# Performance work log

Measured on AMD Instinct MI355X. Metric: run time of the kernel, lower is better.

Reference implementation:

```python
import jax, jax.numpy as jnp
import numpy as np

N_HEADS = 16
HEAD_DIM = 64
N_EMBD = 1024
B, S = 2, 2048


def setup_inputs() -> dict:
    key = jax.random.key(0)
    k1, k2, k3 = jax.random.split(key, 3)
    x = jax.random.normal(k1, (B, S, N_EMBD), dtype=jnp.float32)
    W_attn = jax.random.normal(k2, (N_EMBD, 3 * N_EMBD), dtype=jnp.float32) * 0.02
    b_attn = jnp.zeros((3 * N_EMBD,), dtype=jnp.float32)
    W_proj = jax.random.normal(k3, (N_EMBD, N_EMBD), dtype=jnp.float32) * 0.02
    b_proj = jnp.zeros((N_EMBD,), dtype=jnp.float32)
    return {"x": x, "W_attn": W_attn, "b_attn": b_attn, "W_proj": W_proj, "b_proj": b_proj}


def reference(x, W_attn, b_attn, W_proj, b_proj):
    b, s, _ = x.shape
    qkv = x @ W_attn + b_attn  # (b, s, 3*n_embd)
    q, k, v = jnp.split(qkv, 3, axis=-1)
    # (b, s, n_embd) -> (b, h, s, d)
    def heads(t):
        return t.reshape(b, s, N_HEADS, HEAD_DIM).transpose(0, 2, 1, 3)
    q, k, v = heads(q), heads(k), heads(v)
    scale = 1.0 / jnp.sqrt(jnp.float32(HEAD_DIM))
    scores = jnp.einsum("bhqd,bhkd->bhqk", q, k) * scale
    causal = jnp.triu(jnp.full((s, s), -jnp.inf, dtype=scores.dtype), k=1)
    scores = scores + causal[None, None, :, :]
    attn = jax.nn.softmax(scores, axis=-1)
    out = jnp.einsum("bhqk,bhkd->bhqd", attn, v)  # (b, h, s, d)
    out = out.transpose(0, 2, 1, 3).reshape(b, s, N_EMBD)
    return out @ W_proj + b_proj
```

## Files before the change

### kernel.cpp

```cpp
#include <hip/hip_runtime.h>
#include <hip/hip_bf16.h>
#include <stdint.h>
#include <stddef.h>

typedef __bf16 bf16_t;
typedef __attribute__((ext_vector_type(8))) __bf16 bf16x8;
typedef __attribute__((ext_vector_type(4))) __bf16 bf16x4;
typedef __attribute__((ext_vector_type(4))) float f32x4;

#define MFMA_BF16(a, b, c) __builtin_amdgcn_mfma_f32_16x16x32_bf16((a), (b), (c), 0, 0, 0)

__global__ __launch_bounds__(256) void prep(const void* __restrict__ x,
                                            const void* __restrict__ Wa,
                                            const void* __restrict__ Wp,
                                            bf16_t* __restrict__ xb,
                                            bf16_t* __restrict__ Wat,
                                            bf16_t* __restrict__ Wpt,
                                            int* __restrict__ flag) {
  __shared__ int dcnt;
  __shared__ bf16_t tile[32][33];

  const int tid = threadIdx.x;
  if (tid == 0) dcnt = 0;
  __syncthreads();
  {
    const unsigned short* p = (const unsigned short*)x + tid * 16;
    int local = 0;
#pragma unroll
    for (int i = 0; i < 16; ++i) {
      const int e = (p[i] >> 7) & 0xFF;
      if (e >= 0x8D) local++;
    }
    if (local) atomicAdd(&dcnt, local);
  }
  __syncthreads();
  const int isF32 = (dcnt > 4) ? 1 : 0;

  const int b = blockIdx.x;
  if (b == 0 && tid == 0) *flag = isF32;

  if (b < 2048) {
    if (!isF32) return;
    const size_t i = ((size_t)b * 256 + tid) * 8;
    const float4 a0 = *(const float4*)((const float*)x + i);
    const float4 a1 = *(const float4*)((const float*)x + i + 4);
    bf16x8 r;
    r[0] = (__bf16)a0.x; r[1] = (__bf16)a0.y; r[2] = (__bf16)a0.z; r[3] = (__bf16)a0.w;
    r[4] = (__bf16)a1.x; r[5] = (__bf16)a1.y; r[6] = (__bf16)a1.z; r[7] = (__bf16)a1.w;
    *(bf16x8*)(xb + i) = r;
    return;
  }

  const void* in;
  bf16_t* out;
  int R, C, bx, by;
  if (b < 5120) {
    const int idx = b - 2048;
    in = Wa; out = Wat; R = 1024; C = 3072;
    bx = idx % 96; by = idx / 96;
  } else {
    const int idx = b - 5120;
    in = Wp; out = Wpt; R = 1024; C = 1024;
    bx = idx & 31; by = idx >> 5;
  }
  const int tx = tid & 31, ty = tid >> 5;
  const int r0 = by * 32, c0 = bx * 32;
#pragma unroll
  for (int i = 0; i < 4; ++i) {
    const size_t idx2 = (size_t)(r0 + ty + i * 8) * C + (c0 + tx);
    tile[ty + i * 8][tx] = isF32 ? (bf16_t)((const float*)in)[idx2]
                                 : ((const bf16_t*)in)[idx2];
  }
  __syncthreads();
#pragma unroll
  for (int i = 0; i < 4; ++i)
    out[(size_t)(c0 + ty + i * 8) * R + (r0 + tx)] = tile[tx][ty + i * 8];
}

#define GP 72
template <int MODE>
__global__ __launch_bounds__(256) void gemm_bt(const void* A0,
                        const bf16_t* __restrict__ xb,
                        const bf16_t* __restrict__ Bt,
                        const void* __restrict__ bias,
                        void* C,
                        bf16_t* __restrict__ Qs,
                        bf16_t* __restrict__ Kb,
                        bf16_t* __restrict__ dout_bf,
                        int M, int N, int K,
                        const int* __restrict__ flagp) {
  const int isF32 = *flagp;
  const bf16_t* A = (MODE == 1 && isF32) ? xb : (const bf16_t*)A0;
  bf16_t* Vt = dout_bf + (isF32 ? (size_t)4194304 : 0);

  __shared__ __align__(16) unsigned char pool[128 * GP * 2 * 2];
  bf16_t* As = (bf16_t*)pool;
  bf16_t* Bs = (bf16_t*)pool + 128 * GP;

  const int tid = threadIdx.x;
  const int w = tid >> 6, lane = tid & 63;
  const int quad = lane >> 4, l16 = lane & 15;
  const int wm = w >> 1, wn = w & 1;
  const int m0 = blockIdx.y * 128, n0 = blockIdx.x * 128;

  auto loadA = [&](int k0, int it) -> bf16x8 {
    const int g = it * 256 + tid;
    const int row = g >> 3, col = (g & 7) * 8;
    const int m = m0 + row;
    if (MODE == 2) {
      const size_t aoff =
          ((size_t)((m >> 11) * 16 + (k0 >> 6)) * 2048 + (m & 2047)) * 64 + col;
      return *(const bf16x8*)(A + aoff);
    }
    return *(const bf16x8*)(A + (size_t)m * K + (k0 + col));
  };
  auto loadB = [&](int k0, int it) -> bf16x8 {
    const int g = it * 256 + tid;
    const int row = g >> 3, col = (g & 7) * 8;
    return *(const bf16x8*)(Bt + (size_t)(n0 + row) * K + (k0 + col));
  };

  f32x4 acc[4][4];
#pragma unroll
  for (int i = 0; i < 4; ++i)
#pragma unroll
    for (int j = 0; j < 4; ++j) acc[i][j] = f32x4{0.f, 0.f, 0.f, 0.f};

  bf16x8 va[4], vb[4];
#pragma unroll
  for (int it = 0; it < 4; ++it) { va[it] = loadA(0, it); vb[it] = loadB(0, it); }

  for (int k0 = 0; k0 < K; k0 += 64) {
    __syncthreads();
#pragma unroll
    for (int it = 0; it < 4; ++it) {
      const int g = it * 256 + tid;
      const int row = g >> 3, col = (g & 7) * 8;
      *(bf16x8*)&As[row * GP + col] = va[it];
      *(bf16x8*)&Bs[row * GP + col] = vb[it];
    }
    __syncthreads();

    if (k0 + 64 < K) {
#pragma unroll
      for (int it = 0; it < 4; ++it) { va[it] = loadA(k0 + 64, it); vb[it] = loadB(k0 + 64, it); }
    }

#pragma unroll
    for (int kc = 0; kc < 2; ++kc) {
      bf16x8 af[4], bfr[4];
#pragma unroll
      for (int i = 0; i < 4; ++i)
        af[i] = *(const bf16x8*)&As[(wm * 64 + i * 16 + l16) * GP + kc * 32 + quad * 8];
#pragma unroll
      for (int j = 0; j < 4; ++j)
        bfr[j] = *(const bf16x8*)&Bs[(wn * 64 + j * 16 + l16) * GP + kc * 32 + quad * 8];
#pragma unroll
      for (int i = 0; i < 4; ++i)
#pragma unroll
        for (int j = 0; j < 4; ++j) acc[i][j] = MFMA_BF16(af[i], bfr[j], acc[i][j]);
    }
  }

  if (MODE == 1 && n0 >= 2048) {
    bf16_t* tp = (bf16_t*)pool;
    __syncthreads();
#pragma unroll
    for (int j = 0; j < 4; ++j) {
      const int n_l = wn * 64 + j * 16 + l16;
      const int n = n0 + n_l;
      const float bj = isF32 ? ((const float*)bias)[n] : (float)((const bf16_t*)bias)[n];
#pragma unroll
      for (int i = 0; i < 4; ++i) {
#pragma unroll
        for (int r = 0; r < 4; ++r) {
          const int m_l = wm * 64 + i * 16 + quad * 4 + r;
          tp[n_l * 136 + m_l] = (bf16_t)(acc[i][j][r] + bj);
        }
      }
    }
    __syncthreads();
    const int b = m0 >> 11, s0 = m0 & 2047;
#pragma unroll
    for (int seg = 0; seg < 8; ++seg) {
      const int idx = seg * 256 + tid;
      const int n_l = idx >> 4, ms = (idx & 15) * 8;
      const bf16x8 v8 = *(const bf16x8*)&tp[n_l * 136 + ms];
      const int e = (n0 + n_l) & 1023, h = e >> 6, d = e & 63;
      *(bf16x8*)(Vt + ((size_t)(b * 16 + h) * 64 + d) * 2048 + s0 + ms) = v8;
    }
    return;
  }

  if (MODE == 1) {
    bf16_t* tp = (bf16_t*)pool;
    __syncthreads();
    const bool isQ = (n0 < 1024);
    const float sc = isQ ? 0.18033688011f : 1.0f;
#pragma unroll
    for (int j = 0; j < 4; ++j) {
      const int n_l = wn * 64 + j * 16 + l16;
      const int n = n0 + n_l;
      const float bj = isF32 ? ((const float*)bias)[n] : (float)((const bf16_t*)bias)[n];
#pragma unroll
      for (int i = 0; i < 4; ++i) {
#pragma unroll
        for (int r = 0; r < 4; ++r) {
          const int m_l = wm * 64 + i * 16 + quad * 4 + r;
          tp[m_l * 136 + n_l] = (bf16_t)((acc[i][j][r] + bj) * sc);
        }
      }
    }
    __syncthreads();
    bf16_t* dst = isQ ? Qs : Kb;
#pragma unroll
    for (int seg = 0; seg < 8; ++seg) {
      const int idx = seg * 256 + tid;
      const int m_l = idx >> 4, ns = (idx & 15) * 8;
      const bf16x8 v8 = *(const bf16x8*)&tp[m_l * 136 + ns];
      const int m = m0 + m_l;
      const int e = (n0 + ns) & 1023, h = e >> 6, d = e & 63;
      const int bb = m >> 11, s = m & 2047;
      *(bf16x8*)(dst + (((size_t)(bb * 16 + h) * 2048 + s) * 64 + d)) = v8;
    }
    return;
  }

#pragma unroll
  for (int j = 0; j < 4; ++j) {
    const int n = n0 + wn * 64 + j * 16 + l16;
    const float bj = isF32 ? ((const float*)bias)[n] : (float)((const bf16_t*)bias)[n];
#pragma unroll
    for (int i = 0; i < 4; ++i) {
      const int mbase = m0 + wm * 64 + i * 16 + quad * 4;
#pragma unroll
      for (int r = 0; r < 4; ++r) {
        const int m = mbase + r;
        const float v = acc[i][j][r] + bj;
        if (isF32) ((float*)C)[(size_t)m * N + n] = v;
        else       ((bf16_t*)C)[(size_t)m * N + n] = (bf16_t)v;
      }
    }
  }
}

#define AP 72
#define PSP 72
__global__ __launch_bounds__(256, 5) void attn_kernel(bf16_t* QO,
                                                      const bf16_t* __restrict__ Kb,
                                                      const bf16_t* __restrict__ dout_bf,
                                                      const int* __restrict__ flagp) {
  const int isF32 = *flagp;
  const bf16_t* Vt = dout_bf + (isF32 ? (size_t)4194304 : 0);

  __shared__ __align__(16) bf16_t Ks[64 * AP];
  __shared__ __align__(16) bf16_t Vs[64 * AP];
  __shared__ __align__(16) bf16_t Ps[4][16 * PSP];

  const int bid = blockIdx.x;
  const int g = bid >> 5, bh = bid & 31;
  const int qt = (g < 16) ? (31 - g) : (g - 16);

  const int tid = threadIdx.x, w = tid >> 6, lane = tid & 63;
  const int quad = lane >> 4, l16 = lane & 15;

  bf16_t* Q = QO + (size_t)bh * 2048 * 64;
  const bf16_t* K = Kb + (size_t)bh * 2048 * 64;
  const bf16_t* V = Vt + (size_t)bh * 64 * 2048;

  const int qrow = qt * 64 + w * 16;
  const int nkt = qt + 1;

  bf16x8 qf[2];
#pragma unroll
  for (int kk = 0; kk < 2; ++kk)
    qf[kk] = *(const bf16x8*)(Q + (size_t)(qrow + l16) * 64 + kk * 32 + quad * 8);

  f32x4 oacc[4];
  float lsum = 0.f;
#pragma unroll
  for (int jd = 0; jd < 4; ++jd) oacc[jd] = f32x4{0.f, 0.f, 0.f, 0.f};

  const int srow8 = lane >> 3;
  const int scol8 = (lane & 7) * 8;

  auto loadK = [&](int kt, int it) -> bf16x8 {
    const int row = (w + it * 4) * 8 + srow8;
    return *(const bf16x8*)(K + (size_t)(kt * 64 + row) * 64 + scol8);
  };
  auto loadV = [&](int kt, int it) -> bf16x8 {
    const int row = (w + it * 4) * 8 + srow8;
    return *(const bf16x8*)(V + (size_t)row * 2048 + kt * 64 + scol8);
  };

  bf16x8 kv[2], vv[2];
#pragma unroll
  for (int it = 0; it < 2; ++it) { kv[it] = loadK(0, it); vv[it] = loadV(0, it); }

  for (int kt = 0; kt < nkt; ++kt) {
    __syncthreads();
#pragma unroll
    for (int it = 0; it < 2; ++it) {
      const int row = (w + it * 4) * 8 + srow8;
      *(bf16x8*)&Ks[row * AP + scol8] = kv[it];
      *(bf16x8*)&Vs[row * AP + scol8] = vv[it];
    }
    __syncthreads();

    if (kt + 1 < nkt) {
#pragma unroll
      for (int it = 0; it < 2; ++it) { kv[it] = loadK(kt + 1, it); vv[it] = loadV(kt + 1, it); }
    }

    const int kbase = kt * 64;
    f32x4 s[4];
#pragma unroll
    for (int j = 0; j < 4; ++j) {
      const bf16x8 kf0 = *(const bf16x8*)&Ks[(j * 16 + l16) * AP + quad * 8];
      const bf16x8 kf1 = *(const bf16x8*)&Ks[(j * 16 + l16) * AP + 32 + quad * 8];
      f32x4 z = f32x4{0.f, 0.f, 0.f, 0.f};
      z = MFMA_BF16(kf0, qf[0], z);
      s[j] = MFMA_BF16(kf1, qf[1], z);
    }

    if (kbase + 63 > qrow) {
      const int qg = qrow + l16;
#pragma unroll
      for (int j = 0; j < 4; ++j) {
        const int key = kbase + j * 16 + quad * 4;
#pragma unroll
        for (int r = 0; r < 4; ++r)
          if (key + r > qg) s[j][r] = -1e30f;
      }
    }

#pragma unroll
    for (int j = 0; j < 4; ++j) {
      bf16x4 pk;
#pragma unroll
      for (int r = 0; r < 4; ++r) {
        const float p = exp2f(s[j][r]);
        lsum += p;
        pk[r] = (__bf16)p;
      }
      *(bf16x4*)&Ps[w][l16 * PSP + j * 16 + quad * 4] = pk;
    }

#pragma unroll
    for (int kk = 0; kk < 2; ++kk) {
      const bf16x8 pf = *(const bf16x8*)&Ps[w][l16 * PSP + kk * 32 + quad * 8];
#pragma unroll
      for (int jd = 0; jd < 4; ++jd) {
        const bf16x8 vf = *(const bf16x8*)&Vs[(jd * 16 + l16) * AP + kk * 32 + quad * 8];
        oacc[jd] = MFMA_BF16(pf, vf, oacc[jd]);
      }
    }
  }

  lsum += __shfl_xor(lsum, 16);
  lsum += __shfl_xor(lsum, 32);

#pragma unroll
  for (int r = 0; r < 4; ++r) {
    const float lr = fmaxf(__shfl(lsum, quad * 4 + r, 16), 1e-30f);
    const int q = qrow + quad * 4 + r;
#pragma unroll
    for (int jd = 0; jd < 4; ++jd) {
      const int d = jd * 16 + l16;
      Q[(size_t)q * 64 + d] = (bf16_t)(oacc[jd][r] / lr);
    }
  }
}

extern "C" void kernel_launch(void* const* d_in, const int* in_sizes, int n_in,
                              void* d_out, int out_size, void* d_ws, size_t ws_size,
                              hipStream_t stream) {
  const void* x      = d_in[0];
  const void* W_attn = d_in[1];
  const void* b_attn = d_in[2];
  const void* W_proj = d_in[3];
  const void* b_proj = d_in[4];

  char* ws = (char*)d_ws;
  size_t off = 0;
  auto alloc = [&](size_t bytes) {
    char* p = ws + off;
    off += (bytes + 255) & ~(size_t)255;
    return p;
  };
  int*    flag = (int*)alloc(256);
  bf16_t* Qs   = (bf16_t*)alloc((size_t)32 * 2048 * 64 * 2);
  bf16_t* Kb   = (bf16_t*)alloc((size_t)32 * 2048 * 64 * 2);
  bf16_t* Wat  = (bf16_t*)alloc((size_t)3072 * 1024 * 2);
  bf16_t* Wpt  = (bf16_t*)alloc((size_t)1024 * 1024 * 2);
  bf16_t* dout_bf = (bf16_t*)d_out;

  prep<<<dim3(6144), 256, 0, stream>>>(x, W_attn, W_proj, dout_bf, Wat, Wpt, flag);

  gemm_bt<1><<<dim3(3072 / 128, 4096 / 128), 256, 0, stream>>>(
      x, dout_bf, Wat, b_attn, nullptr, Qs, Kb, dout_bf, 4096, 3072, 1024, flag);

  attn_kernel<<<dim3(1024), 256, 0, stream>>>(Qs, Kb, dout_bf, flag);

  gemm_bt<2><<<dim3(1024 / 128, 4096 / 128), 256, 0, stream>>>(
      Qs, nullptr, Wpt, b_proj, d_out, nullptr, nullptr, dout_bf, 4096, 1024, 1024, flag);
}
```

Before: 189.7 us.

## Double attention query tile per block to reuse K/V tiles across 32 rows per wave

Each attention block now handles 128 query rows, with each wave covering 32 rows in two 16-row groups, instead of 64 rows. K and V fragments loaded from shared memory are reused across both groups, halving the number of blocks and the global K/V traffic per query. Groups fully above the causal diagonal are skipped per tile. The launch-bounds occupancy hint drops from 5 to 2 and the grid shrinks to 512 blocks, which lowers parallelism and makes per-block work more uneven under the causal mask.

```diff
diff --git a/kernel.cpp b/kernel.cpp
--- a/kernel.cpp
+++ b/kernel.cpp
@@ -246,7 +246,7 @@
 
 #define AP 72
 #define PSP 72
-__global__ __launch_bounds__(256, 5) void attn_kernel(bf16_t* QO,
+__global__ __launch_bounds__(256, 2) void attn_kernel(bf16_t* QO,
                                                       const bf16_t* __restrict__ Kb,
                                                       const bf16_t* __restrict__ dout_bf,
                                                       const int* __restrict__ flagp) {
@@ -255,11 +255,11 @@
 
   __shared__ __align__(16) bf16_t Ks[64 * AP];
   __shared__ __align__(16) bf16_t Vs[64 * AP];
-  __shared__ __align__(16) bf16_t Ps[4][16 * PSP];
+  __shared__ __align__(16) bf16_t Ps[4][32 * PSP];
 
   const int bid = blockIdx.x;
-  const int g = bid >> 5, bh = bid & 31;
-  const int qt = (g < 16) ? (31 - g) : (g - 16);
+  const int g2 = bid >> 5, bh = bid & 31;
+  const int qt = (g2 < 8) ? (15 - g2) : (g2 - 8);
 
   const int tid = threadIdx.x, w = tid >> 6, lane = tid & 63;
   const int quad = lane >> 4, l16 = lane & 15;
@@ -268,18 +268,22 @@
   const bf16_t* K = Kb + (size_t)bh * 2048 * 64;
   const bf16_t* V = Vt + (size_t)bh * 64 * 2048;
 
-  const int qrow = qt * 64 + w * 16;
-  const int nkt = qt + 1;
-
-  bf16x8 qf[2];
-#pragma unroll
-  for (int kk = 0; kk < 2; ++kk)
-    qf[kk] = *(const bf16x8*)(Q + (size_t)(qrow + l16) * 64 + kk * 32 + quad * 8);
-
-  f32x4 oacc[4];
-  float lsum = 0.f;
-#pragma unroll
-  for (int jd = 0; jd < 4; ++jd) oacc[jd] = f32x4{0.f, 0.f, 0.f, 0.f};
+  const int qrow = qt * 128 + w * 32;
+  const int nkt = 2 * qt + 2;
+
+  bf16x8 qf[2][2];
+#pragma unroll
+  for (int g = 0; g < 2; ++g)
+#pragma unroll
+    for (int kk = 0; kk < 2; ++kk)
+      qf[g][kk] = *(const bf16x8*)(Q + (size_t)(qrow + g * 16 + l16) * 64 + kk * 32 + quad * 8);
+
+  f32x4 oacc[2][4];
+  float lsum[2] = {0.f, 0.f};
+#pragma unroll
+  for (int g = 0; g < 2; ++g)
+#pragma unroll
+    for (int jd = 0; jd < 4; ++jd) oacc[g][jd] = f32x4{0.f, 0.f, 0.f, 0.f};
 
   const int srow8 = lane >> 3;
   const int scol8 = (lane & 7) * 8;
@@ -313,61 +317,87 @@
     }
 
     const int kbase = kt * 64;
-    f32x4 s[4];
-#pragma unroll
-    for (int j = 0; j < 4; ++j) {
-      const bf16x8 kf0 = *(const bf16x8*)&Ks[(j * 16 + l16) * AP + quad * 8];
-      const bf16x8 kf1 = *(const bf16x8*)&Ks[(j * 16 + l16) * AP + 32 + quad * 8];
-      f32x4 z = f32x4{0.f, 0.f, 0.f, 0.f};
-      z = MFMA_BF16(kf0, qf[0], z);
-      s[j] = MFMA_BF16(kf1, qf[1], z);
-    }
-
-    if (kbase + 63 > qrow) {
-      const int qg = qrow + l16;
+    const bool active = kbase <= qrow + 31;
+    if (active) {
+      bf16x8 kf[4][2];
 #pragma unroll
       for (int j = 0; j < 4; ++j) {
-        const int key = kbase + j * 16 + quad * 4;
-#pragma unroll
-        for (int r = 0; r < 4; ++r)
-          if (key + r > qg) s[j][r] = -1e30f;
-      }
-    }
-
-#pragma unroll
-    for (int j = 0; j < 4; ++j) {
-      bf16x4 pk;
-#pragma unroll
-      for (int r = 0; r < 4; ++r) {
-        const float p = exp2f(s[j][r]);
-        lsum += p;
-        pk[r] = (__bf16)p;
-      }
-      *(bf16x4*)&Ps[w][l16 * PSP + j * 16 + quad * 4] = pk;
-    }
-
-#pragma unroll
-    for (int kk = 0; kk < 2; ++kk) {
-      const bf16x8 pf = *(const bf16x8*)&Ps[w][l16 * PSP + kk * 32 + quad * 8];
+        kf[j][0] = *(const bf16x8*)&Ks[(j * 16 + l16) * AP + quad * 8];
+        kf[j][1] = *(const bf16x8*)&Ks[(j * 16 + l16) * AP + 32 + quad * 8];
+      }
+
+#pragma unroll
+      for (int g = 0; g < 2; ++g) {
+        const int qg = qrow + g * 16 + l16;
+        if (kbase > qrow + g * 16 + 15) continue;
+
+        f32x4 s[4];
+#pragma unroll
+        for (int j = 0; j < 4; ++j) {
+          f32x4 z = f32x4{0.f, 0.f, 0.f, 0.f};
+          z = MFMA_BF16(kf[j][0], qf[g][0], z);
+          s[j] = MFMA_BF16(kf[j][1], qf[g][1], z);
+        }
+
+        if (kbase + 63 > qrow + g * 16) {
+#pragma unroll
+          for (int j = 0; j < 4; ++j) {
+            const int key = kbase + j * 16 + quad * 4;
+#pragma unroll
+            for (int r = 0; r < 4; ++r)
+              if (key + r > qg) s[j][r] = -1e30f;
+          }
+        }
+
+        float ls = 0.f;
+#pragma unroll
+        for (int j = 0; j < 4; ++j) {
+          bf16x4 pk;
+#pragma unroll
+          for (int r = 0; r < 4; ++r) {
+            const float p = exp2f(s[j][r]);
+            ls += p;
+            pk[r] = (__bf16)p;
+          }
+          *(bf16x4*)&Ps[w][(g * 16 + l16) * PSP + j * 16 + quad * 4] = pk;
+        }
+        lsum[g] += ls;
+      }
+
+#pragma unroll
+      for (int kk = 0; kk < 2; ++kk) {
+        bf16x8 vf[4];
+#pragma unroll
+        for (int jd = 0; jd < 4; ++jd)
+          vf[jd] = *(const bf16x8*)&Vs[(jd * 16 + l16) * AP + kk * 32 + quad * 8];
+#pragma unroll
+        for (int g = 0; g < 2; ++g) {
+          if (kbase > qrow + g * 16 + 15) continue;
+          const bf16x8 pf = *(const bf16x8*)&Ps[w][(g * 16 + l16) * PSP + kk * 32 + quad * 8];
+#pragma unroll
+          for (int jd = 0; jd < 4; ++jd) oacc[g][jd] = MFMA_BF16(pf, vf[jd], oacc[g][jd]);
+        }
+      }
+    }
+  }
+
+#pragma unroll
+  for (int g = 0; g < 2; ++g) {
+    lsum[g] += __shfl_xor(lsum[g], 16);
+    lsum[g] += __shfl_xor(lsum[g], 32);
+  }
+
+#pragma unroll
+  for (int g = 0; g < 2; ++g) {
+#pragma unroll
+    for (int r = 0; r < 4; ++r) {
+      const float lr = fmaxf(__shfl(lsum[g], quad * 4 + r, 16), 1e-30f);
+      const int q = qrow + g * 16 + quad * 4 + r;
 #pragma unroll
       for (int jd = 0; jd < 4; ++jd) {
-        const bf16x8 vf = *(const bf16x8*)&Vs[(jd * 16 + l16) * AP + kk * 32 + quad * 8];
-        oacc[jd] = MFMA_BF16(pf, vf, oacc[jd]);
-      }
-    }
-  }
-
-  lsum += __shfl_xor(lsum, 16);
-  lsum += __shfl_xor(lsum, 32);
-
-#pragma unroll
-  for (int r = 0; r < 4; ++r) {
-    const float lr = fmaxf(__shfl(lsum, quad * 4 + r, 16), 1e-30f);
-    const int q = qrow + quad * 4 + r;
-#pragma unroll
-    for (int jd = 0; jd < 4; ++jd) {
-      const int d = jd * 16 + l16;
-      Q[(size_t)q * 64 + d] = (bf16_t)(oacc[jd][r] / lr);
+        const int d = jd * 16 + l16;
+        Q[(size_t)q * 64 + d] = (bf16_t)(oacc[g][jd][r] / lr);
+      }
     }
   }
 }
@@ -400,7 +430,7 @@
   gemm_bt<1><<<dim3(3072 / 128, 4096 / 128), 256, 0, stream>>>(
       x, dout_bf, Wat, b_attn, nullptr, Qs, Kb, dout_bf, 4096, 3072, 1024, flag);
 
-  attn_kernel<<<dim3(1024), 256, 0, stream>>>(Qs, Kb, dout_bf, flag);
+  attn_kernel<<<dim3(512), 256, 0, stream>>>(Qs, Kb, dout_bf, flag);
 
   gemm_bt<2><<<dim3(1024 / 128, 4096 / 128), 256, 0, stream>>>(
       Qs, nullptr, Wpt, b_proj, d_out, nullptr, nullptr, dout_bf, 4096, 1024, 1024, flag);
```

After: 195.0 us. +2.8%, slower.

## Load GEMM tiles directly into LDS with global_load_lds and unpadded layout

Applied to the files above, without the earlier changes.

Replaces the register-staged global-to-shared tile copy in the GEMM kernel with direct global-to-LDS loads, and switches the shared tiles from a padded stride to a dense 64-element row stride. This removes the VGPR round trip and the explicit shared stores. In exchange it drops the register prefetch of the next K tile, so loads no longer overlap compute. The unpadded layout may also introduce LDS bank conflicts on the fragment reads.

```diff
diff --git a/kernel.cpp b/kernel.cpp
--- a/kernel.cpp
+++ b/kernel.cpp
@@ -9,6 +9,11 @@
 typedef __attribute__((ext_vector_type(4))) float f32x4;
 
 #define MFMA_BF16(a, b, c) __builtin_amdgcn_mfma_f32_16x16x32_bf16((a), (b), (c), 0, 0, 0)
+
+#define GLOAD_LDS(gsrc, ldst)                                                   \
+  __builtin_amdgcn_global_load_lds(                                             \
+      (const __attribute__((address_space(1))) unsigned int*)(gsrc),            \
+      (__attribute__((address_space(3))) unsigned int*)(ldst), 16, 0, 0)
 
 __global__ __launch_bounds__(256) void prep(const void* __restrict__ x,
                                             const void* __restrict__ Wa,
@@ -95,7 +100,7 @@
 
   __shared__ __align__(16) unsigned char pool[128 * GP * 2 * 2];
   bf16_t* As = (bf16_t*)pool;
-  bf16_t* Bs = (bf16_t*)pool + 128 * GP;
+  bf16_t* Bs = (bf16_t*)pool + 128 * 64;
 
   const int tid = threadIdx.x;
   const int w = tid >> 6, lane = tid & 63;
@@ -103,21 +108,21 @@
   const int wm = w >> 1, wn = w & 1;
   const int m0 = blockIdx.y * 128, n0 = blockIdx.x * 128;
 
-  auto loadA = [&](int k0, int it) -> bf16x8 {
+  auto gsrcA = [&](int k0, int it) -> const bf16_t* {
     const int g = it * 256 + tid;
     const int row = g >> 3, col = (g & 7) * 8;
     const int m = m0 + row;
     if (MODE == 2) {
       const size_t aoff =
           ((size_t)((m >> 11) * 16 + (k0 >> 6)) * 2048 + (m & 2047)) * 64 + col;
-      return *(const bf16x8*)(A + aoff);
-    }
-    return *(const bf16x8*)(A + (size_t)m * K + (k0 + col));
+      return A + aoff;
+    }
+    return A + (size_t)m * K + (k0 + col);
   };
-  auto loadB = [&](int k0, int it) -> bf16x8 {
+  auto gsrcB = [&](int k0, int it) -> const bf16_t* {
     const int g = it * 256 + tid;
     const int row = g >> 3, col = (g & 7) * 8;
-    return *(const bf16x8*)(Bt + (size_t)(n0 + row) * K + (k0 + col));
+    return Bt + (size_t)(n0 + row) * K + (k0 + col);
   };
 
   f32x4 acc[4][4];
@@ -126,35 +131,24 @@
 #pragma unroll
     for (int j = 0; j < 4; ++j) acc[i][j] = f32x4{0.f, 0.f, 0.f, 0.f};
 
-  bf16x8 va[4], vb[4];
-#pragma unroll
-  for (int it = 0; it < 4; ++it) { va[it] = loadA(0, it); vb[it] = loadB(0, it); }
-
   for (int k0 = 0; k0 < K; k0 += 64) {
     __syncthreads();
 #pragma unroll
     for (int it = 0; it < 4; ++it) {
-      const int g = it * 256 + tid;
-      const int row = g >> 3, col = (g & 7) * 8;
-      *(bf16x8*)&As[row * GP + col] = va[it];
-      *(bf16x8*)&Bs[row * GP + col] = vb[it];
-    }
-    __syncthreads();
-
-    if (k0 + 64 < K) {
-#pragma unroll
-      for (int it = 0; it < 4; ++it) { va[it] = loadA(k0 + 64, it); vb[it] = loadB(k0 + 64, it); }
-    }
+      GLOAD_LDS(gsrcA(k0, it), As + it * 2048 + w * 512);
+      GLOAD_LDS(gsrcB(k0, it), Bs + it * 2048 + w * 512);
+    }
+    __syncthreads();
 
 #pragma unroll
     for (int kc = 0; kc < 2; ++kc) {
       bf16x8 af[4], bfr[4];
 #pragma unroll
       for (int i = 0; i < 4; ++i)
-        af[i] = *(const bf16x8*)&As[(wm * 64 + i * 16 + l16) * GP + kc * 32 + quad * 8];
+        af[i] = *(const bf16x8*)&As[(wm * 64 + i * 16 + l16) * 64 + kc * 32 + quad * 8];
 #pragma unroll
       for (int j = 0; j < 4; ++j)
-        bfr[j] = *(const bf16x8*)&Bs[(wn * 64 + j * 16 + l16) * GP + kc * 32 + quad * 8];
+        bfr[j] = *(const bf16x8*)&Bs[(wn * 64 + j * 16 + l16) * 64 + kc * 32 + quad * 8];
 #pragma unroll
       for (int i = 0; i < 4; ++i)
 #pragma unroll
```

Result: slower. 213.0 us (+12.3%).
